# Kernel optimization log

Hardware: AMD Instinct MI355X
Metric: run time of the kernel (lower is better)

Reference implementation:

```python
import jax, jax.numpy as jnp
import numpy as np

D_MODEL, D_STATE, D_CONV, D_INNER, DT_RANK, K = 96, 16, 3, 192, 6, 4
B, H, W = 1, 64, 64


def setup_inputs() -> dict:
    key = jax.random.key(0)
    ks = jax.random.split(key, 10)
    x = jax.random.normal(ks[0], (B, H, W, D_MODEL), jnp.float32)
    in_proj_w = jax.random.normal(ks[1], (2 * D_INNER, D_MODEL), jnp.float32) * 0.02
    conv_w = jax.random.normal(ks[2], (D_INNER, 1, D_CONV, D_CONV), jnp.float32) * 0.1
    conv_b = jnp.zeros((D_INNER,), jnp.float32)
    x_proj_w = jax.random.normal(ks[3], (K, DT_RANK + 2 * D_STATE, D_INNER), jnp.float32) * 0.02
    dt_std = DT_RANK ** -0.5
    dt_w = jax.random.uniform(ks[4], (K, D_INNER, DT_RANK), jnp.float32, -dt_std, dt_std)
    # dt bias init: inv-softplus of dt ~ logUniform(1e-3, 1e-1)
    u = jax.random.uniform(ks[5], (K, D_INNER), jnp.float32)
    dt = jnp.exp(u * (np.log(0.1) - np.log(0.001)) + np.log(0.001)).clip(1e-4)
    dt_b = dt + jnp.log(-jnp.expm1(-dt))
    A_logs = jnp.log(jnp.broadcast_to(jnp.arange(1, D_STATE + 1, dtype=jnp.float32), (K * D_INNER, D_STATE)))
    Ds = jnp.ones((K * D_INNER,), jnp.float32)
    ln_g = jnp.ones((D_INNER,), jnp.float32)
    ln_b = jnp.zeros((D_INNER,), jnp.float32)
    out_proj_w = jax.random.normal(ks[6], (D_MODEL, D_INNER), jnp.float32) * 0.02
    return dict(x=x, in_proj_w=in_proj_w, conv_w=conv_w, conv_b=conv_b, x_proj_w=x_proj_w,
                dt_w=dt_w, dt_b=dt_b, A_logs=A_logs, Ds=Ds, ln_g=ln_g, ln_b=ln_b,
                out_proj_w=out_proj_w)


def _ss2d(x, in_proj_w, conv_w, conv_b, x_proj_w, dt_w, dt_b, A_logs, Ds, ln_g, ln_b, out_proj_w):
    b, h, w, c = x.shape
    L = h * w
    d = conv_w.shape[0]            # d_inner
    n = A_logs.shape[1]            # d_state
    r = dt_w.shape[2]              # dt_rank
    # in_proj + split
    xz = jnp.einsum('bhwc,ec->bhwe', x, in_proj_w)
    xx, z = xz[..., :d], xz[..., d:]
    # depthwise conv (NCHW) + SiLU
    xc = xx.transpose(0, 3, 1, 2)
    pad = (D_CONV - 1) // 2
    xc = jax.lax.conv_general_dilated(xc, conv_w, (1, 1), [(pad, pad), (pad, pad)],
                                      feature_group_count=d) + conv_b[None, :, None, None]
    xc = jax.nn.silu(xc)
    # 4 scan directions: HW, WH, and their reverses
    x_hw = xc.reshape(b, d, L)
    x_wh = xc.transpose(0, 1, 3, 2).reshape(b, d, L)
    xs = jnp.stack([x_hw, x_wh, x_hw[..., ::-1], x_wh[..., ::-1]], axis=1)  # (b,K,d,L)
    x_dbl = jnp.einsum('bkdl,kcd->bkcl', xs, x_proj_w)
    dts, Bs, Cs = x_dbl[:, :, :r], x_dbl[:, :, r:r + n], x_dbl[:, :, r + n:]
    dts = jnp.einsum('bkrl,kdr->bkdl', dts, dt_w)
    delta = jax.nn.softplus(dts + dt_b[None, :, :, None])        # (b,K,d,L)
    A = -jnp.exp(A_logs).reshape(K, d, n)
    # time-major scanned inputs
    dA = jnp.exp(jnp.einsum('bkdl,kdn->lbkdn', delta, A))        # (L,b,K,d,n)
    dBu = jnp.einsum('bkdl,bknl,bkdl->lbkdn', delta, Bs, xs)
    Ct = Cs.transpose(3, 0, 1, 2)                                # (L,b,K,n)
    def step(hst, inp):
        dA_t, dBu_t, C_t = inp
        hst = dA_t * hst + dBu_t
        return hst, jnp.einsum('bkdn,bkn->bkd', hst, C_t)
    h0 = jnp.zeros((b, K, d, n), jnp.float32)
    _, ys = jax.lax.scan(step, h0, (dA, dBu, Ct))                # ys: (L,b,K,d)
    out_y = ys.transpose(1, 2, 3, 0) + xs * Ds.reshape(K, d)[None, :, :, None]
    # recombine directions
    inv = out_y[:, 2:4][..., ::-1]
    y1 = out_y[:, 0]
    y2 = inv[:, 0]
    wh = out_y[:, 1].reshape(b, d, w, h).transpose(0, 1, 3, 2).reshape(b, d, L)
    invwh = inv[:, 1].reshape(b, d, w, h).transpose(0, 1, 3, 2).reshape(b, d, L)
    y = (y1 + y2 + wh + invwh).transpose(0, 2, 1).reshape(b, h, w, d)
    # LayerNorm (eps=1e-5, torch default)
    mu = y.mean(-1, keepdims=True)
    var = ((y - mu) ** 2).mean(-1, keepdims=True)
    y = (y - mu) * jax.lax.rsqrt(var + 1e-5) * ln_g + ln_b
    y = y * jax.nn.silu(z)
    return jnp.einsum('bhwd,cd->bhwc', y, out_proj_w)


def reference(x, in_proj_w, conv_w, conv_b, x_proj_w, dt_w, dt_b, A_logs, Ds, ln_g, ln_b, out_proj_w):
    return _ss2d(x, in_proj_w, conv_w, conv_b, x_proj_w, dt_w, dt_b, A_logs, Ds, ln_g, ln_b, out_proj_w)
```

## Files before the change

kernel.cpp:

```cpp
#include <hip/hip_runtime.h>
#include <hip/hip_bf16.h>

#define LL 4096
#define DM 96
#define DI 192
#define NS 16
#define RK 6
#define RKP 8
#define KD 4
#define CPROJ 38
#define NC (KD*DI*NS)
#define PT 32
#define WS 196
#define OT 16
#define L2E 1.44269504f

__device__ __forceinline__ float b2f(__hip_bfloat16 v){ return __bfloat162float(v); }

__device__ __forceinline__ int detect_bf16(const unsigned short* __restrict__ xh, int tid, int* sflag){
  if (tid < 64){
    unsigned short u = xh[2*tid];
    int e = (u >> 7) & 0xFF;
    int sane = (e >= 107 && e <= 131) ? 1 : 0;
    unsigned long long m = __ballot(sane);
    if (tid == 0) *sflag = (__popcll(m) >= 32) ? 1 : 0;
  }
  return 0;
}

struct P12 { const void* p[12]; };
__global__ void k_convert_all(P12 ptrs, float* __restrict__ dst) {
  const int off[12] = {0,36864,38592,38784,67968,72576,73344,85632,86400,86592,86784,105216};
  __shared__ int sflag;
  detect_bf16((const unsigned short*)ptrs.p[0], threadIdx.x, &sflag);
  __syncthreads();
  int f = sflag;
  int i = blockIdx.x * 256 + threadIdx.x;
  if (i >= 105216) return;
  int j = 0;
  #pragma unroll
  for (int s = 1; s < 11; s++) if (i >= off[s]) j = s;
  int e = i - off[j];
  const void* src = ptrs.p[j+1];
  if (f) dst[i] = b2f(((const __hip_bfloat16*)src)[e]);
  else   dst[i] = ((const float*)src)[e];
}

__global__ void k_inproj(const void* __restrict__ xraw,
                         const float* __restrict__ w,
                         float* __restrict__ xx, float* __restrict__ z) {
  __shared__ float xr[8*DM];
  __shared__ int sflag;
  int tid = threadIdx.x;
  detect_bf16((const unsigned short*)xraw, tid, &sflag);
  __syncthreads();
  int l0 = blockIdx.x * 8;
  if (sflag){
    const __hip_bfloat16* xb = (const __hip_bfloat16*)xraw + (size_t)l0*DM;
    for (int i = tid; i < 8*DM; i += 384) xr[i] = b2f(xb[i]);
  } else {
    const float* xf = (const float*)xraw + (size_t)l0*DM;
    for (int i = tid; i < 8*DM; i += 384) xr[i] = xf[i];
  }
  __syncthreads();
  int e = tid;
  float acc[8];
  #pragma unroll
  for (int i=0;i<8;i++) acc[i]=0.f;
  const float* wr = w + e*DM;
  for (int c=0;c<DM;c++){
    float wv = wr[c];
    #pragma unroll
    for (int i=0;i<8;i++) acc[i] = fmaf(wv, xr[i*DM+c], acc[i]);
  }
  if (e < DI) {
    #pragma unroll
    for (int i=0;i<8;i++) xx[(l0+i)*DI + e] = acc[i];
  } else {
    int e2 = e - DI;
    #pragma unroll
    for (int i=0;i<8;i++) z[(l0+i)*DI + e2] = acc[i];
  }
}

__global__ void k_conv(const float* __restrict__ xx,
                       const float* __restrict__ cw,
                       const float* __restrict__ cb,
                       float* __restrict__ xc,
                       float* __restrict__ xct) {
  int l = blockIdx.x;
  int d = threadIdx.x;
  int h = l >> 6, w = l & 63;
  float acc = cb[d];
  #pragma unroll
  for (int ki=0; ki<3; ki++){
    int hh = h + ki - 1;
    if ((unsigned)hh >= 64u) continue;
    #pragma unroll
    for (int kj=0;kj<3;kj++){
      int wj = w + kj - 1;
      if ((unsigned)wj >= 64u) continue;
      acc = fmaf(cw[d*9 + ki*3 + kj], xx[(hh*64+wj)*DI + d], acc);
    }
  }
  float v = acc / (1.f + __expf(-acc));
  xc[l*DI + d] = v;
  xct[(((w<<6)|h))*DI + d] = v;
}

__device__ __forceinline__ int dir_map(int k, int t){
  if (k==0) return t;
  if (k==1) return ((t&63)<<6) | (t>>6);
  if (k==2) return 4095 - t;
  int u = 4095 - t; return ((u&63)<<6) | (u>>6);
}

__global__ void __launch_bounds__(256) k_proj(const float* __restrict__ xc,
                       const float* __restrict__ xpw,
                       float* __restrict__ dts,
                       float* __restrict__ Bb, float* __restrict__ Cb) {
  __shared__ float wl[CPROJ*WS];
  __shared__ float xs[PT*WS];
  int b = blockIdx.x;
  int k = b >> 7;
  int t_base = (b & 127) * PT;
  int tid = threadIdx.x;
  for (int idx = tid; idx < CPROJ*DI; idx += 256){
    int cc = idx / DI, j = idx - cc*DI;
    wl[cc*WS + j] = xpw[(k*CPROJ + cc)*DI + j];
  }
  for (int idx = tid; idx < PT*DI; idx += 256){
    int tt = idx / DI, j = idx - tt*DI;
    xs[tt*WS + j] = xc[dir_map(k, t_base + tt)*DI + j];
  }
  __syncthreads();
  int tg = tid & 7;
  int ty = tid >> 3;
  int cc0 = ty;
  int has2 = (ty + 32 < CPROJ);
  int cc1 = has2 ? (ty + 32) : ty;
  float a0x=0.f,a0y=0.f,a0z=0.f,a0w=0.f;
  float a1x=0.f,a1y=0.f,a1z=0.f,a1w=0.f;
  const float4* w0p = (const float4*)&wl[cc0*WS];
  const float4* w1p = (const float4*)&wl[cc1*WS];
  const float4* x0p = (const float4*)&xs[(tg     )*WS];
  const float4* x1p = (const float4*)&xs[(tg +  8)*WS];
  const float4* x2p = (const float4*)&xs[(tg + 16)*WS];
  const float4* x3p = (const float4*)&xs[(tg + 24)*WS];
  #pragma unroll 4
  for (int jc = 0; jc < DI/4; jc++){
    float4 w0 = w0p[jc], w1 = w1p[jc];
    float4 x0 = x0p[jc], x1 = x1p[jc], x2 = x2p[jc], x3 = x3p[jc];
    a0x = fmaf(w0.x,x0.x,fmaf(w0.y,x0.y,fmaf(w0.z,x0.z,fmaf(w0.w,x0.w,a0x))));
    a0y = fmaf(w0.x,x1.x,fmaf(w0.y,x1.y,fmaf(w0.z,x1.z,fmaf(w0.w,x1.w,a0y))));
    a0z = fmaf(w0.x,x2.x,fmaf(w0.y,x2.y,fmaf(w0.z,x2.z,fmaf(w0.w,x2.w,a0z))));
    a0w = fmaf(w0.x,x3.x,fmaf(w0.y,x3.y,fmaf(w0.z,x3.z,fmaf(w0.w,x3.w,a0w))));
    a1x = fmaf(w1.x,x0.x,fmaf(w1.y,x0.y,fmaf(w1.z,x0.z,fmaf(w1.w,x0.w,a1x))));
    a1y = fmaf(w1.x,x1.x,fmaf(w1.y,x1.y,fmaf(w1.z,x1.z,fmaf(w1.w,x1.w,a1y))));
    a1z = fmaf(w1.x,x2.x,fmaf(w1.y,x2.y,fmaf(w1.z,x2.z,fmaf(w1.w,x2.w,a1z))));
    a1w = fmaf(w1.x,x3.x,fmaf(w1.y,x3.y,fmaf(w1.z,x3.z,fmaf(w1.w,x3.w,a1w))));
  }
  float accs0[4] = {a0x,a0y,a0z,a0w};
  float accs1[4] = {a1x,a1y,a1z,a1w};
  #pragma unroll
  for (int i=0;i<4;i++){
    int t = t_base + tg + 8*i;
    size_t kt = (size_t)k*LL + t;
    {
      int cc = cc0; float v = accs0[i];
      if (cc < RK)            dts[kt*RKP + cc] = v;
      else if (cc < RK+NS)    Bb [kt*NS + (cc-RK)] = v;
      else                    Cb [kt*NS + (cc-RK-NS)] = v;
    }
    if (has2){
      int cc = ty + 32; float v = accs1[i];
      if (cc < RK+NS)         Bb [kt*NS + (cc-RK)] = v;
      else                    Cb [kt*NS + (cc-RK-NS)] = v;
    }
  }
}

template<int CHB>
__global__ void __launch_bounds__(256) k_scan1(
                      const float* __restrict__ xc_hw,
                      const float* __restrict__ xc_wh,
                      const float* __restrict__ dts,
                      const float* __restrict__ Bbuf,
                      const float* __restrict__ Cbuf,
                      const float* __restrict__ A_logs,
                      const float* __restrict__ dtw,
                      const float* __restrict__ dtb,
                      float* __restrict__ PH,
                      float* __restrict__ SDb,
                      float* __restrict__ ydir) {
  constexpr int CS = LL >> CHB;
  int b = blockIdx.x;
  int c = b & ((1<<CHB)-1);
  int kg = b >> CHB;
  int k = kg / 3, dg3 = kg - k*3;
  int tid = threadIdx.x;
  int dl = tid >> 2, nq = tid & 3;
  int d = dg3*64 + dl;
  int kd = k*DI + d;
  float4 Al = *(const float4*)&A_logs[kd*NS + nq*4];
  float A0 = -__expf(Al.x)*L2E, A1 = -__expf(Al.y)*L2E;
  float A2 = -__expf(Al.z)*L2E, A3 = -__expf(Al.w)*L2E;
  float bt = dtb[kd];
  float w0 = dtw[kd*RK+0], w1 = dtw[kd*RK+1], w2 = dtw[kd*RK+2];
  float w3 = dtw[kd*RK+3], w4 = dtw[kd*RK+4], w5 = dtw[kd*RK+5];
  const float* dr = dts + ((size_t)k*LL + c*CS)*RKP;
  const float4* bp = (const float4*)(Bbuf + ((size_t)k*LL + c*CS)*NS) + nq;
  const float4* cp = (const float4*)(Cbuf + ((size_t)k*LL + c*CS)*NS) + nq;
  const float* xbase = (k & 1) ? xc_wh : xc_hw;
  int l0 = (k < 2) ? (c*CS) : (4095 - c*CS);
  int lstep = (k < 2) ? DI : -DI;
  const float* xp = xbase + (size_t)l0*DI + d;
  float* yp = ydir + ((size_t)k*LL + c*CS)*DI + d;
  float* sdp = SDb + ((size_t)k*LL + c*CS)*DI + d;
  float h0=0.f,h1=0.f,h2=0.f,h3=0.f, cumD=0.f;
  #pragma unroll
  for (int s=0; s<CS; s++){
    float4 lo = *(const float4*)(dr + s*RKP);
    float4 hi = *(const float4*)(dr + s*RKP + 4);
    float v = bt;
    v = fmaf(w0, lo.x, v); v = fmaf(w1, lo.y, v); v = fmaf(w2, lo.z, v);
    v = fmaf(w3, lo.w, v); v = fmaf(w4, hi.x, v); v = fmaf(w5, hi.y, v);
    float sp = (v > 20.f) ? v : __logf(1.f + __expf(v));
    cumD += sp;
    float sx = sp * xp[(ptrdiff_t)s*lstep];
    float4 bv = bp[s*4];
    float4 cv = cp[s*4];
    float a;
    a = exp2f(sp*A0); h0 = fmaf(a, h0, sx*bv.x);
    a = exp2f(sp*A1); h1 = fmaf(a, h1, sx*bv.y);
    a = exp2f(sp*A2); h2 = fmaf(a, h2, sx*bv.z);
    a = exp2f(sp*A3); h3 = fmaf(a, h3, sx*bv.w);
    float y = h0*cv.x + h1*cv.y + h2*cv.z + h3*cv.w;
    y += __shfl_xor(y, 1, 64);
    y += __shfl_xor(y, 2, 64);
    if (nq == 0){
      yp[s*DI] = y;
      sdp[s*DI] = cumD;
    }
  }
  size_t base2 = ((size_t)c*NC + kd*NS + nq*4)*2;
  *(float4*)&PH[base2]   = make_float4(exp2f(A0*cumD), h0, exp2f(A1*cumD), h1);
  *(float4*)&PH[base2+4] = make_float4(exp2f(A2*cumD), h2, exp2f(A3*cumD), h3);
}

template<int CHB>
__global__ void __launch_bounds__(256) k_scan2(float2* __restrict__ PH) {
  constexpr int CH = 1 << CHB;
  int idx = blockIdx.x*256 + threadIdx.x;
  float h = 0.f;
  #pragma unroll 8
  for (int c=0;c<CH;c++){
    float2 ph = PH[(size_t)c*NC + idx];
    PH[(size_t)c*NC + idx].y = h;
    h = fmaf(ph.x, h, ph.y);
  }
}

template<int CHB>
__global__ void __launch_bounds__(192) k_corr(
                      const float* __restrict__ Cbuf,
                      const float* __restrict__ A_logs,
                      const float2* __restrict__ PH,
                      const float* __restrict__ SDb,
                      float* __restrict__ ydir) {
  constexpr int CS = LL >> CHB;
  int b = blockIdx.x;
  int k = b >> CHB;
  int c = b & ((1<<CHB)-1);
  if (c == 0) return;
  int t0 = c*CS;
  int d = threadIdx.x;
  int kd = k*DI + d;
  __shared__ float cs[CS*NS];
  for (int i = d; i < CS*NS; i += 192)
    cs[i] = Cbuf[((size_t)k*LL + t0)*NS + i];
  float A2[16], he[16];
  {
    const float4* ap = (const float4*)&A_logs[kd*NS];
    const float2* hp = PH + (size_t)c*NC + kd*NS;
    #pragma unroll
    for (int i=0;i<4;i++){
      float4 av = ap[i];
      A2[4*i+0] = -__expf(av.x)*L2E; A2[4*i+1] = -__expf(av.y)*L2E;
      A2[4*i+2] = -__expf(av.z)*L2E; A2[4*i+3] = -__expf(av.w)*L2E;
    }
    #pragma unroll
    for (int n=0;n<16;n++) he[n] = hp[n].y;
  }
  __syncthreads();
  float* yp = ydir + ((size_t)k*LL + t0)*DI + d;
  const float* sdp = SDb + ((size_t)k*LL + t0)*DI + d;
  #pragma unroll 4
  for (int s=0; s<CS; s++){
    float SD = sdp[s*DI];
    float corr = 0.f;
    #pragma unroll
    for (int n=0;n<16;n++)
      corr = fmaf(cs[s*NS+n]*exp2f(A2[n]*SD), he[n], corr);
    yp[s*DI] += corr;
  }
}

__global__ void __launch_bounds__(192) k_out(
                      const float* __restrict__ ydir,
                      const float* __restrict__ xc,
                      const float* __restrict__ z,
                      const float* __restrict__ Ds,
                      const float* __restrict__ ln_g,
                      const float* __restrict__ ln_b,
                      const float* __restrict__ opw,
                      void* __restrict__ out,
                      const unsigned short* __restrict__ xh) {
  __shared__ float gs[OT*WS];
  __shared__ float ps[2][OT][12];
  __shared__ float mv[2][OT];
  __shared__ int sflag;
  int tid = threadIdx.x;
  int d = tid;
  detect_bf16(xh, tid, &sflag);
  int l0 = blockIdx.x * OT;
  float dsum = Ds[d] + Ds[DI+d] + Ds[2*DI+d] + Ds[3*DI+d];
  #pragma unroll 4
  for (int r=0;r<OT;r++){
    int l = l0 + r;
    int lt = ((l & 63) << 6) | (l >> 6);
    float y = ydir[(size_t)l*DI + d]
            + ydir[((size_t)LL   + lt)*DI + d]
            + ydir[((size_t)2*LL + (4095 - l))*DI + d]
            + ydir[((size_t)3*LL + (4095 - lt))*DI + d];
    gs[r*WS + d] = fmaf(xc[(size_t)l*DI + d], dsum, y);
  }
  __syncthreads();
  {
    int r = tid / 12, lane = tid - r*12;
    float s1 = 0.f, s2 = 0.f;
    for (int j = lane; j < DI; j += 12){
      float v = gs[r*WS + j];
      s1 += v; s2 += v*v;
    }
    ps[0][r][lane] = s1; ps[1][r][lane] = s2;
  }
  __syncthreads();
  if (tid < OT){
    float a = 0.f, bb = 0.f;
    #pragma unroll
    for (int j=0;j<12;j++){ a += ps[0][tid][j]; bb += ps[1][tid][j]; }
    float mu = a * (1.f/192.f);
    float var = bb * (1.f/192.f) - mu*mu;
    mv[0][tid] = mu; mv[1][tid] = rsqrtf(var + 1e-5f);
  }
  __syncthreads();
  float lg = ln_g[d], lb = ln_b[d];
  #pragma unroll 4
  for (int r=0;r<OT;r++){
    float yn = (gs[r*WS + d] - mv[0][r]) * mv[1][r] * lg + lb;
    float zv = z[(size_t)(l0+r)*DI + d];
    gs[r*WS + d] = yn * (zv / (1.f + __expf(-zv)));
  }
  __syncthreads();
  int half = tid / 96;
  int e = tid - half*96;
  int r0 = half*8;
  float acc[8];
  #pragma unroll
  for (int i=0;i<8;i++) acc[i] = 0.f;
  const float4* wrow = (const float4*)(opw + e*DI);
  #pragma unroll 4
  for (int jc = 0; jc < DI/4; jc++){
    float4 w = wrow[jc];
    #pragma unroll
    for (int i=0;i<8;i++){
      float4 gv = *(const float4*)&gs[(r0+i)*WS + jc*4];
      acc[i] = fmaf(w.x,gv.x,fmaf(w.y,gv.y,fmaf(w.z,gv.z,fmaf(w.w,gv.w,acc[i]))));
    }
  }
  int f = sflag;
  #pragma unroll
  for (int i=0;i<8;i++){
    int l = l0 + r0 + i;
    if (f) ((__hip_bfloat16*)out)[l*DM + e] = __float2bfloat16(acc[i]);
    else   ((float*)out)[l*DM + e] = acc[i];
  }
}

extern "C" void kernel_launch(void* const* d_in, const int* in_sizes, int n_in,
                              void* d_out, int out_size, void* d_ws, size_t ws_size,
                              hipStream_t stream) {
  float* ws = (float*)d_ws;
  float* cvt = ws + 16;
  const int off[12] = {0,36864,38592,38784,67968,72576,73344,85632,86400,86592,86784,105216};
  float* c[12];
  c[0] = nullptr;
  for (int i = 1; i < 12; i++) c[i] = cvt + off[i-1];

  float* big    = cvt + 105216;
  float* xx     = big;
  float* z      = xx + (size_t)LL*DI;
  float* xc     = z  + (size_t)LL*DI;
  float* xct    = xc + (size_t)LL*DI;
  float* dts    = xct + (size_t)LL*DI;
  float* Bb     = dts + (size_t)KD*LL*RKP;
  float* Cb     = Bb + (size_t)KD*LL*NS;
  float* PH     = Cb + (size_t)KD*LL*NS;
  size_t need128 = (size_t)(16 + 105216 + 4*786432 + 131072 + 2*262144
                            + 2*128*NC + 2*(size_t)KD*LL*DI) * 4;
  int chBits = (ws_size >= need128) ? 7 : 6;
  int CHn = 1 << chBits;
  float* SDb  = PH + 2*(size_t)CHn*NC;
  float* ydir = SDb + (size_t)KD*LL*DI;

  P12 ptrs;
  for (int i = 0; i < 12; i++) ptrs.p[i] = d_in[i];
  k_convert_all<<<(105216 + 255)/256, 256, 0, stream>>>(ptrs, cvt);

  k_inproj<<<LL/8, 384, 0, stream>>>(d_in[0], c[1], xx, z);
  k_conv<<<LL, DI, 0, stream>>>(xx, c[2], c[3], xc, xct);
  k_proj<<<KD*(LL/PT), 256, 0, stream>>>(xc, c[4], dts, Bb, Cb);
  if (chBits == 7){
    k_scan1<7><<<KD*3*128, 256, 0, stream>>>(xc, xct, dts, Bb, Cb, c[7], c[5], c[6],
                                             PH, SDb, ydir);
    k_scan2<7><<<NC/256, 256, 0, stream>>>((float2*)PH);
    k_corr<7><<<KD*128, 192, 0, stream>>>(Cb, c[7], (const float2*)PH, SDb, ydir);
  } else {
    k_scan1<6><<<KD*3*64, 256, 0, stream>>>(xc, xct, dts, Bb, Cb, c[7], c[5], c[6],
                                            PH, SDb, ydir);
    k_scan2<6><<<NC/256, 256, 0, stream>>>((float2*)PH);
    k_corr<6><<<KD*64, 192, 0, stream>>>(Cb, c[7], (const float2*)PH, SDb, ydir);
  }
  k_out<<<LL/OT, 192, 0, stream>>>(ydir, xc, z, c[8], c[9], c[10], c[11], d_out,
                                   (const unsigned short*)d_in[0]);
}
```

Baseline: 202.8 us.

## Drop weight conversion kernel, read raw params inline and recompute cumulative dt

Removes the separate kernel that converted all parameters to fp32 in workspace; each kernel now detects the input dtype and converts parameters on load. The scan no longer writes a per-step cumulative-dt buffer; the correction kernel recomputes softplus(dt) from the projected dts instead. The in-projection tile also grows from 8 to 16 rows. This saves a launch and a large write/read of the cumulative-dt array, at the cost of repeated dtype detection per block and extra softplus arithmetic in the correction pass.

```diff
diff --git a/kernel.cpp b/kernel.cpp
--- a/kernel.cpp
+++ b/kernel.cpp
@@ -13,11 +13,17 @@
 #define PT 32
 #define WS 196
 #define OT 16
+#define IT 16
 #define L2E 1.44269504f
 
-__device__ __forceinline__ float b2f(__hip_bfloat16 v){ return __bfloat162float(v); }
-
-__device__ __forceinline__ int detect_bf16(const unsigned short* __restrict__ xh, int tid, int* sflag){
+__device__ __forceinline__ float bu(unsigned short u){
+  return __uint_as_float(((unsigned int)u) << 16);
+}
+__device__ __forceinline__ float ldp(const void* p, size_t i, int f){
+  return f ? bu(((const unsigned short*)p)[i]) : ((const float*)p)[i];
+}
+
+__device__ __forceinline__ void detect_bf16(const unsigned short* __restrict__ xh, int tid, int* sflag){
   if (tid < 64){
     unsigned short u = xh[2*tid];
     int e = (u >> 7) & 0xFF;
@@ -25,73 +31,69 @@
     unsigned long long m = __ballot(sane);
     if (tid == 0) *sflag = (__popcll(m) >= 32) ? 1 : 0;
   }
-  return 0;
-}
-
-struct P12 { const void* p[12]; };
-__global__ void k_convert_all(P12 ptrs, float* __restrict__ dst) {
-  const int off[12] = {0,36864,38592,38784,67968,72576,73344,85632,86400,86592,86784,105216};
-  __shared__ int sflag;
-  detect_bf16((const unsigned short*)ptrs.p[0], threadIdx.x, &sflag);
-  __syncthreads();
-  int f = sflag;
-  int i = blockIdx.x * 256 + threadIdx.x;
-  if (i >= 105216) return;
-  int j = 0;
-  #pragma unroll
-  for (int s = 1; s < 11; s++) if (i >= off[s]) j = s;
-  int e = i - off[j];
-  const void* src = ptrs.p[j+1];
-  if (f) dst[i] = b2f(((const __hip_bfloat16*)src)[e]);
-  else   dst[i] = ((const float*)src)[e];
-}
-
-__global__ void k_inproj(const void* __restrict__ xraw,
-                         const float* __restrict__ w,
+}
+
+__global__ void __launch_bounds__(384) k_inproj(const void* __restrict__ xraw,
+                         const void* __restrict__ wraw,
                          float* __restrict__ xx, float* __restrict__ z) {
-  __shared__ float xr[8*DM];
+  __shared__ float xr[IT*DM];
   __shared__ int sflag;
   int tid = threadIdx.x;
   detect_bf16((const unsigned short*)xraw, tid, &sflag);
   __syncthreads();
-  int l0 = blockIdx.x * 8;
-  if (sflag){
-    const __hip_bfloat16* xb = (const __hip_bfloat16*)xraw + (size_t)l0*DM;
-    for (int i = tid; i < 8*DM; i += 384) xr[i] = b2f(xb[i]);
+  int f = sflag;
+  int l0 = blockIdx.x * IT;
+  if (f){
+    const unsigned short* xb = (const unsigned short*)xraw + (size_t)l0*DM;
+    for (int i = tid; i < IT*DM; i += 384) xr[i] = bu(xb[i]);
   } else {
     const float* xf = (const float*)xraw + (size_t)l0*DM;
-    for (int i = tid; i < 8*DM; i += 384) xr[i] = xf[i];
+    for (int i = tid; i < IT*DM; i += 384) xr[i] = xf[i];
   }
   __syncthreads();
   int e = tid;
-  float acc[8];
-  #pragma unroll
-  for (int i=0;i<8;i++) acc[i]=0.f;
-  const float* wr = w + e*DM;
-  for (int c=0;c<DM;c++){
-    float wv = wr[c];
-    #pragma unroll
-    for (int i=0;i<8;i++) acc[i] = fmaf(wv, xr[i*DM+c], acc[i]);
+  float acc[IT];
+  #pragma unroll
+  for (int i=0;i<IT;i++) acc[i]=0.f;
+  if (f){
+    const unsigned short* wr = (const unsigned short*)wraw + (size_t)e*DM;
+    for (int c=0;c<DM;c++){
+      float wv = bu(wr[c]);
+      #pragma unroll
+      for (int i=0;i<IT;i++) acc[i] = fmaf(wv, xr[i*DM+c], acc[i]);
+    }
+  } else {
+    const float* wr = (const float*)wraw + (size_t)e*DM;
+    for (int c=0;c<DM;c++){
+      float wv = wr[c];
+      #pragma unroll
+      for (int i=0;i<IT;i++) acc[i] = fmaf(wv, xr[i*DM+c], acc[i]);
+    }
   }
   if (e < DI) {
     #pragma unroll
-    for (int i=0;i<8;i++) xx[(l0+i)*DI + e] = acc[i];
+    for (int i=0;i<IT;i++) xx[(size_t)(l0+i)*DI + e] = acc[i];
   } else {
     int e2 = e - DI;
     #pragma unroll
-    for (int i=0;i<8;i++) z[(l0+i)*DI + e2] = acc[i];
+    for (int i=0;i<IT;i++) z[(size_t)(l0+i)*DI + e2] = acc[i];
   }
 }
 
 __global__ void k_conv(const float* __restrict__ xx,
-                       const float* __restrict__ cw,
-                       const float* __restrict__ cb,
+                       const void* __restrict__ cw,
+                       const void* __restrict__ cb,
                        float* __restrict__ xc,
-                       float* __restrict__ xct) {
+                       float* __restrict__ xct,
+                       const unsigned short* __restrict__ xh) {
+  __shared__ int sflag;
   int l = blockIdx.x;
   int d = threadIdx.x;
+  detect_bf16(xh, d, &sflag);
+  __syncthreads();
+  int f = sflag;
   int h = l >> 6, w = l & 63;
-  float acc = cb[d];
+  float acc = ldp(cb, d, f);
   #pragma unroll
   for (int ki=0; ki<3; ki++){
     int hh = h + ki - 1;
@@ -100,7 +102,7 @@
     for (int kj=0;kj<3;kj++){
       int wj = w + kj - 1;
       if ((unsigned)wj >= 64u) continue;
-      acc = fmaf(cw[d*9 + ki*3 + kj], xx[(hh*64+wj)*DI + d], acc);
+      acc = fmaf(ldp(cw, d*9 + ki*3 + kj, f), xx[(hh*64+wj)*DI + d], acc);
     }
   }
   float v = acc / (1.f + __expf(-acc));
@@ -116,18 +118,23 @@
 }
 
 __global__ void __launch_bounds__(256) k_proj(const float* __restrict__ xc,
-                       const float* __restrict__ xpw,
+                       const void* __restrict__ xpw,
                        float* __restrict__ dts,
-                       float* __restrict__ Bb, float* __restrict__ Cb) {
+                       float* __restrict__ Bb, float* __restrict__ Cb,
+                       const unsigned short* __restrict__ xh) {
   __shared__ float wl[CPROJ*WS];
   __shared__ float xs[PT*WS];
+  __shared__ int sflag;
   int b = blockIdx.x;
   int k = b >> 7;
   int t_base = (b & 127) * PT;
   int tid = threadIdx.x;
+  detect_bf16(xh, tid, &sflag);
+  __syncthreads();
+  int f = sflag;
   for (int idx = tid; idx < CPROJ*DI; idx += 256){
     int cc = idx / DI, j = idx - cc*DI;
-    wl[cc*WS + j] = xpw[(k*CPROJ + cc)*DI + j];
+    wl[cc*WS + j] = ldp(xpw, (size_t)(k*CPROJ + cc)*DI + j, f);
   }
   for (int idx = tid; idx < PT*DI; idx += 256){
     int tt = idx / DI, j = idx - tt*DI;
@@ -187,27 +194,33 @@
                       const float* __restrict__ dts,
                       const float* __restrict__ Bbuf,
                       const float* __restrict__ Cbuf,
-                      const float* __restrict__ A_logs,
-                      const float* __restrict__ dtw,
-                      const float* __restrict__ dtb,
+                      const void* __restrict__ A_logs,
+                      const void* __restrict__ dtw,
+                      const void* __restrict__ dtb,
                       float* __restrict__ PH,
-                      float* __restrict__ SDb,
-                      float* __restrict__ ydir) {
+                      float* __restrict__ ydir,
+                      const unsigned short* __restrict__ xh) {
   constexpr int CS = LL >> CHB;
+  __shared__ int sflag;
   int b = blockIdx.x;
   int c = b & ((1<<CHB)-1);
   int kg = b >> CHB;
   int k = kg / 3, dg3 = kg - k*3;
   int tid = threadIdx.x;
+  detect_bf16(xh, tid, &sflag);
+  __syncthreads();
+  int f = sflag;
   int dl = tid >> 2, nq = tid & 3;
   int d = dg3*64 + dl;
   int kd = k*DI + d;
-  float4 Al = *(const float4*)&A_logs[kd*NS + nq*4];
-  float A0 = -__expf(Al.x)*L2E, A1 = -__expf(Al.y)*L2E;
-  float A2 = -__expf(Al.z)*L2E, A3 = -__expf(Al.w)*L2E;
-  float bt = dtb[kd];
-  float w0 = dtw[kd*RK+0], w1 = dtw[kd*RK+1], w2 = dtw[kd*RK+2];
-  float w3 = dtw[kd*RK+3], w4 = dtw[kd*RK+4], w5 = dtw[kd*RK+5];
+  float A0 = -__expf(ldp(A_logs, (size_t)kd*NS + nq*4 + 0, f))*L2E;
+  float A1 = -__expf(ldp(A_logs, (size_t)kd*NS + nq*4 + 1, f))*L2E;
+  float A2 = -__expf(ldp(A_logs, (size_t)kd*NS + nq*4 + 2, f))*L2E;
+  float A3 = -__expf(ldp(A_logs, (size_t)kd*NS + nq*4 + 3, f))*L2E;
+  float bt = ldp(dtb, kd, f);
+  float w0 = ldp(dtw, (size_t)kd*RK+0, f), w1 = ldp(dtw, (size_t)kd*RK+1, f);
+  float w2 = ldp(dtw, (size_t)kd*RK+2, f), w3 = ldp(dtw, (size_t)kd*RK+3, f);
+  float w4 = ldp(dtw, (size_t)kd*RK+4, f), w5 = ldp(dtw, (size_t)kd*RK+5, f);
   const float* dr = dts + ((size_t)k*LL + c*CS)*RKP;
   const float4* bp = (const float4*)(Bbuf + ((size_t)k*LL + c*CS)*NS) + nq;
   const float4* cp = (const float4*)(Cbuf + ((size_t)k*LL + c*CS)*NS) + nq;
@@ -216,7 +229,6 @@
   int lstep = (k < 2) ? DI : -DI;
   const float* xp = xbase + (size_t)l0*DI + d;
   float* yp = ydir + ((size_t)k*LL + c*CS)*DI + d;
-  float* sdp = SDb + ((size_t)k*LL + c*CS)*DI + d;
   float h0=0.f,h1=0.f,h2=0.f,h3=0.f, cumD=0.f;
   #pragma unroll
   for (int s=0; s<CS; s++){
@@ -238,12 +250,9 @@
     float y = h0*cv.x + h1*cv.y + h2*cv.z + h3*cv.w;
     y += __shfl_xor(y, 1, 64);
     y += __shfl_xor(y, 2, 64);
-    if (nq == 0){
-      yp[s*DI] = y;
-      sdp[s*DI] = cumD;
-    }
-  }
-  size_t base2 = ((size_t)c*NC + kd*NS + nq*4)*2;
+    if (nq == 0) yp[s*DI] = y;
+  }
+  size_t base2 = ((size_t)c*NC + (size_t)kd*NS + nq*4)*2;
   *(float4*)&PH[base2]   = make_float4(exp2f(A0*cumD), h0, exp2f(A1*cumD), h1);
   *(float4*)&PH[base2+4] = make_float4(exp2f(A2*cumD), h2, exp2f(A3*cumD), h3);
 }
@@ -264,44 +273,57 @@
 template<int CHB>
 __global__ void __launch_bounds__(192) k_corr(
                       const float* __restrict__ Cbuf,
-                      const float* __restrict__ A_logs,
+                      const float* __restrict__ dts,
+                      const void* __restrict__ A_logs,
+                      const void* __restrict__ dtw,
+                      const void* __restrict__ dtb,
                       const float2* __restrict__ PH,
-                      const float* __restrict__ SDb,
-                      float* __restrict__ ydir) {
+                      float* __restrict__ ydir,
+                      const unsigned short* __restrict__ xh) {
   constexpr int CS = LL >> CHB;
+  __shared__ float cs[CS*NS];
+  __shared__ int sflag;
   int b = blockIdx.x;
   int k = b >> CHB;
   int c = b & ((1<<CHB)-1);
+  int d = threadIdx.x;
+  detect_bf16(xh, d, &sflag);
   if (c == 0) return;
   int t0 = c*CS;
-  int d = threadIdx.x;
   int kd = k*DI + d;
-  __shared__ float cs[CS*NS];
   for (int i = d; i < CS*NS; i += 192)
     cs[i] = Cbuf[((size_t)k*LL + t0)*NS + i];
+  __syncthreads();
+  int f = sflag;
+  float bt = ldp(dtb, kd, f);
+  float w0 = ldp(dtw, (size_t)kd*RK+0, f), w1 = ldp(dtw, (size_t)kd*RK+1, f);
+  float w2 = ldp(dtw, (size_t)kd*RK+2, f), w3 = ldp(dtw, (size_t)kd*RK+3, f);
+  float w4 = ldp(dtw, (size_t)kd*RK+4, f), w5 = ldp(dtw, (size_t)kd*RK+5, f);
   float A2[16], he[16];
   {
-    const float4* ap = (const float4*)&A_logs[kd*NS];
-    const float2* hp = PH + (size_t)c*NC + kd*NS;
-    #pragma unroll
-    for (int i=0;i<4;i++){
-      float4 av = ap[i];
-      A2[4*i+0] = -__expf(av.x)*L2E; A2[4*i+1] = -__expf(av.y)*L2E;
-      A2[4*i+2] = -__expf(av.z)*L2E; A2[4*i+3] = -__expf(av.w)*L2E;
-    }
-    #pragma unroll
-    for (int n=0;n<16;n++) he[n] = hp[n].y;
-  }
-  __syncthreads();
+    const float2* hp = PH + (size_t)c*NC + (size_t)kd*NS;
+    #pragma unroll
+    for (int n=0;n<16;n++){
+      A2[n] = -__expf(ldp(A_logs, (size_t)kd*NS + n, f))*L2E;
+      he[n] = hp[n].y;
+    }
+  }
+  const float* dr = dts + ((size_t)k*LL + t0)*RKP;
   float* yp = ydir + ((size_t)k*LL + t0)*DI + d;
-  const float* sdp = SDb + ((size_t)k*LL + t0)*DI + d;
+  float cumD = 0.f;
   #pragma unroll 4
   for (int s=0; s<CS; s++){
-    float SD = sdp[s*DI];
+    float4 lo = *(const float4*)(dr + s*RKP);
+    float4 hi = *(const float4*)(dr + s*RKP + 4);
+    float v = bt;
+    v = fmaf(w0, lo.x, v); v = fmaf(w1, lo.y, v); v = fmaf(w2, lo.z, v);
+    v = fmaf(w3, lo.w, v); v = fmaf(w4, hi.x, v); v = fmaf(w5, hi.y, v);
+    float sp = (v > 20.f) ? v : __logf(1.f + __expf(v));
+    cumD += sp;
     float corr = 0.f;
     #pragma unroll
     for (int n=0;n<16;n++)
-      corr = fmaf(cs[s*NS+n]*exp2f(A2[n]*SD), he[n], corr);
+      corr = fmaf(cs[s*NS+n]*exp2f(A2[n]*cumD), he[n], corr);
     yp[s*DI] += corr;
   }
 }
@@ -310,10 +332,10 @@
                       const float* __restrict__ ydir,
                       const float* __restrict__ xc,
                       const float* __restrict__ z,
-                      const float* __restrict__ Ds,
-                      const float* __restrict__ ln_g,
-                      const float* __restrict__ ln_b,
-                      const float* __restrict__ opw,
+                      const void* __restrict__ Ds,
+                      const void* __restrict__ ln_g,
+                      const void* __restrict__ ln_b,
+                      const void* __restrict__ opw,
                       void* __restrict__ out,
                       const unsigned short* __restrict__ xh) {
   __shared__ float gs[OT*WS];
@@ -323,8 +345,10 @@
   int tid = threadIdx.x;
   int d = tid;
   detect_bf16(xh, tid, &sflag);
+  __syncthreads();
+  int f = sflag;
   int l0 = blockIdx.x * OT;
-  float dsum = Ds[d] + Ds[DI+d] + Ds[2*DI+d] + Ds[3*DI+d];
+  float dsum = ldp(Ds, d, f) + ldp(Ds, DI+d, f) + ldp(Ds, 2*DI+d, f) + ldp(Ds, 3*DI+d, f);
   #pragma unroll 4
   for (int r=0;r<OT;r++){
     int l = l0 + r;
@@ -355,7 +379,7 @@
     mv[0][tid] = mu; mv[1][tid] = rsqrtf(var + 1e-5f);
   }
   __syncthreads();
-  float lg = ln_g[d], lb = ln_b[d];
+  float lg = ldp(ln_g, d, f), lb = ldp(ln_b, d, f);
   #pragma unroll 4
   for (int r=0;r<OT;r++){
     float yn = (gs[r*WS + d] - mv[0][r]) * mv[1][r] * lg + lb;
@@ -369,17 +393,30 @@
   float acc[8];
   #pragma unroll
   for (int i=0;i<8;i++) acc[i] = 0.f;
-  const float4* wrow = (const float4*)(opw + e*DI);
-  #pragma unroll 4
-  for (int jc = 0; jc < DI/4; jc++){
-    float4 w = wrow[jc];
-    #pragma unroll
-    for (int i=0;i<8;i++){
-      float4 gv = *(const float4*)&gs[(r0+i)*WS + jc*4];
-      acc[i] = fmaf(w.x,gv.x,fmaf(w.y,gv.y,fmaf(w.z,gv.z,fmaf(w.w,gv.w,acc[i]))));
-    }
-  }
-  int f = sflag;
+  if (f){
+    const ushort4* wr4 = (const ushort4*)((const unsigned short*)opw + (size_t)e*DI);
+    #pragma unroll 4
+    for (int jc = 0; jc < DI/4; jc++){
+      ushort4 u = wr4[jc];
+      float wx = bu(u.x), wy = bu(u.y), wz = bu(u.z), ww = bu(u.w);
+      #pragma unroll
+      for (int i=0;i<8;i++){
+        float4 gv = *(const float4*)&gs[(r0+i)*WS + jc*4];
+        acc[i] = fmaf(wx,gv.x,fmaf(wy,gv.y,fmaf(wz,gv.z,fmaf(ww,gv.w,acc[i]))));
+      }
+    }
+  } else {
+    const float4* wrow = (const float4*)((const float*)opw + (size_t)e*DI);
+    #pragma unroll 4
+    for (int jc = 0; jc < DI/4; jc++){
+      float4 w = wrow[jc];
+      #pragma unroll
+      for (int i=0;i<8;i++){
+        float4 gv = *(const float4*)&gs[(r0+i)*WS + jc*4];
+        acc[i] = fmaf(w.x,gv.x,fmaf(w.y,gv.y,fmaf(w.z,gv.z,fmaf(w.w,gv.w,acc[i]))));
+      }
+    }
+  }
   #pragma unroll
   for (int i=0;i<8;i++){
     int l = l0 + r0 + i;
@@ -391,15 +428,9 @@
 extern "C" void kernel_launch(void* const* d_in, const int* in_sizes, int n_in,
                               void* d_out, int out_size, void* d_ws, size_t ws_size,
                               hipStream_t stream) {
+  const unsigned short* xh = (const unsigned short*)d_in[0];
   float* ws = (float*)d_ws;
-  float* cvt = ws + 16;
-  const int off[12] = {0,36864,38592,38784,67968,72576,73344,85632,86400,86592,86784,105216};
-  float* c[12];
-  c[0] = nullptr;
-  for (int i = 1; i < 12; i++) c[i] = cvt + off[i-1];
-
-  float* big    = cvt + 105216;
-  float* xx     = big;
+  float* xx     = ws;
   float* z      = xx + (size_t)LL*DI;
   float* xc     = z  + (size_t)LL*DI;
   float* xct    = xc + (size_t)LL*DI;
@@ -407,31 +438,28 @@
   float* Bb     = dts + (size_t)KD*LL*RKP;
   float* Cb     = Bb + (size_t)KD*LL*NS;
   float* PH     = Cb + (size_t)KD*LL*NS;
-  size_t need128 = (size_t)(16 + 105216 + 4*786432 + 131072 + 2*262144
-                            + 2*128*NC + 2*(size_t)KD*LL*DI) * 4;
+  size_t need128 = (size_t)(4*786432 + 131072 + 2*262144
+                            + 2*128*NC + (size_t)KD*LL*DI) * 4;
   int chBits = (ws_size >= need128) ? 7 : 6;
   int CHn = 1 << chBits;
-  float* SDb  = PH + 2*(size_t)CHn*NC;
-  float* ydir = SDb + (size_t)KD*LL*DI;
-
-  P12 ptrs;
-  for (int i = 0; i < 12; i++) ptrs.p[i] = d_in[i];
-  k_convert_all<<<(105216 + 255)/256, 256, 0, stream>>>(ptrs, cvt);
-
-  k_inproj<<<LL/8, 384, 0, stream>>>(d_in[0], c[1], xx, z);
-  k_conv<<<LL, DI, 0, stream>>>(xx, c[2], c[3], xc, xct);
-  k_proj<<<KD*(LL/PT), 256, 0, stream>>>(xc, c[4], dts, Bb, Cb);
+  float* ydir = PH + 2*(size_t)CHn*NC;
+
+  k_inproj<<<LL/IT, 384, 0, stream>>>(d_in[0], d_in[1], xx, z);
+  k_conv<<<LL, DI, 0, stream>>>(xx, d_in[2], d_in[3], xc, xct, xh);
+  k_proj<<<KD*(LL/PT), 256, 0, stream>>>(xc, d_in[4], dts, Bb, Cb, xh);
   if (chBits == 7){
-    k_scan1<7><<<KD*3*128, 256, 0, stream>>>(xc, xct, dts, Bb, Cb, c[7], c[5], c[6],
-                                             PH, SDb, ydir);
+    k_scan1<7><<<KD*3*128, 256, 0, stream>>>(xc, xct, dts, Bb, Cb,
+                                             d_in[7], d_in[5], d_in[6], PH, ydir, xh);
     k_scan2<7><<<NC/256, 256, 0, stream>>>((float2*)PH);
-    k_corr<7><<<KD*128, 192, 0, stream>>>(Cb, c[7], (const float2*)PH, SDb, ydir);
+    k_corr<7><<<KD*128, 192, 0, stream>>>(Cb, dts, d_in[7], d_in[5], d_in[6],
+                                          (const float2*)PH, ydir, xh);
   } else {
-    k_scan1<6><<<KD*3*64, 256, 0, stream>>>(xc, xct, dts, Bb, Cb, c[7], c[5], c[6],
-                                            PH, SDb, ydir);
+    k_scan1<6><<<KD*3*64, 256, 0, stream>>>(xc, xct, dts, Bb, Cb,
+                                            d_in[7], d_in[5], d_in[6], PH, ydir, xh);
     k_scan2<6><<<NC/256, 256, 0, stream>>>((float2*)PH);
-    k_corr<6><<<KD*64, 192, 0, stream>>>(Cb, c[7], (const float2*)PH, SDb, ydir);
-  }
-  k_out<<<LL/OT, 192, 0, stream>>>(ydir, xc, z, c[8], c[9], c[10], c[11], d_out,
-                                   (const unsigned short*)d_in[0]);
-}
+    k_corr<6><<<KD*64, 192, 0, stream>>>(Cb, dts, d_in[7], d_in[5], d_in[6],
+                                         (const float2*)PH, ydir, xh);
+  }
+  k_out<<<LL/OT, 192, 0, stream>>>(ydir, xc, z, d_in[8], d_in[9], d_in[10], d_in[11],
+                                   d_out, xh);
+}
```

After: 223.7 us. 10.3% more time.
